# Kernel optimization log

Hardware: AMD Instinct MI355X
Metric: run time of the kernel (lower is better)

The kernel has to match this reference:

```python
import jax, jax.numpy as jnp
import numpy as np

N, E, F_IN, C, H, B = 50000, 1600000, 64, 64, 2, 64
EPS_BN = 1e-5
NEG_SLOPE = 0.2


def setup_inputs() -> dict:
    key = jax.random.key(0)
    ks = jax.random.split(key, 20)
    s_in = 1.0 / np.sqrt(F_IN)
    s_c = 1.0 / np.sqrt(C)
    inp = {
        "x": jax.random.normal(ks[0], (N, F_IN), jnp.float32),
        "edge_index": jax.random.randint(ks[1], (2, E), 0, N, jnp.int32),
        "batch_index": jnp.sort(jax.random.randint(ks[2], (N,), 0, B, jnp.int32)),
        # GAT layer 1
        "W1": jax.random.normal(ks[3], (F_IN, H * C), jnp.float32) * s_in,
        "att_src1": jax.random.normal(ks[4], (H, C), jnp.float32) * s_c,
        "att_dst1": jax.random.normal(ks[5], (H, C), jnp.float32) * s_c,
        "bias1": jnp.zeros((C,), jnp.float32),
        # skip linear
        "skipW": jax.random.normal(ks[6], (F_IN, C), jnp.float32) * s_in,
        "skipb": jnp.zeros((C,), jnp.float32),
        # BN1
        "gamma1": jnp.ones((C,), jnp.float32),
        "beta1": jnp.zeros((C,), jnp.float32),
        # GAT layer 2
        "W2": jax.random.normal(ks[7], (C, H * C), jnp.float32) * s_c,
        "att_src2": jax.random.normal(ks[8], (H, C), jnp.float32) * s_c,
        "att_dst2": jax.random.normal(ks[9], (H, C), jnp.float32) * s_c,
        "bias2": jnp.zeros((C,), jnp.float32),
        # BN2
        "gamma2": jnp.ones((C,), jnp.float32),
        "beta2": jnp.zeros((C,), jnp.float32),
    }
    return inp


def _gat_conv(x, W, att_src, att_dst, bias, src, dst):
    # PyG GATConv with concat=False (mean over heads), self-loops already in src/dst
    n = x.shape[0]
    h = (x @ W).reshape(n, H, C)                           # [N,H,C]
    a_s = jnp.einsum("nhc,hc->nh", h, att_src)              # [N,H]
    a_d = jnp.einsum("nhc,hc->nh", h, att_dst)
    logits = jax.nn.leaky_relu(a_s[src] + a_d[dst], NEG_SLOPE)  # [E,H]
    m = jax.ops.segment_max(logits, dst, num_segments=n)    # scatter-softmax
    e = jnp.exp(logits - m[dst])
    denom = jax.ops.segment_sum(e, dst, num_segments=n)
    alpha = e / denom[dst]                                  # [E,H]
    msg = h[src] * alpha[:, :, None]                        # [E,H,C]
    out = jax.ops.segment_sum(msg, dst, num_segments=n)     # [N,H,C]
    return out.mean(axis=1) + bias                          # concat=False -> head mean


def _bn(x, gamma, beta):
    # BatchNorm1d, training mode (batch statistics, biased var)
    mu = x.mean(axis=0)
    var = x.var(axis=0)
    return (x - mu) * jax.lax.rsqrt(var + EPS_BN) * gamma + beta


def reference(x, edge_index, batch_index, W1, att_src1, att_dst1, bias1,
              skipW, skipb, gamma1, beta1, W2, att_src2, att_dst2, bias2,
              gamma2, beta2):
    n = x.shape[0]
    loops = jnp.arange(n, dtype=edge_index.dtype)
    src = jnp.concatenate([edge_index[0], loops])  # add_self_loops=True (PyG default)
    dst = jnp.concatenate([edge_index[1], loops])

    h = _gat_conv(x, W1, att_src1, att_dst1, bias1, src, dst)
    h = _bn(h, gamma1, beta1)
    h = jax.nn.gelu(h + x @ skipW + skipb)          # dropout = identity (eval)

    h2 = _gat_conv(h, W2, att_src2, att_dst2, bias2, src, dst)
    h2 = _bn(h2, gamma2, beta2)
    h2 = jax.nn.gelu(h2 + h)

    # global_mean_pool
    sums = jax.ops.segment_sum(h2, batch_index, num_segments=B)
    cnts = jax.ops.segment_sum(jnp.ones((n,), h2.dtype), batch_index, num_segments=B)
    return sums / jnp.maximum(cnts, 1.0)[:, None]   # [B, C]
```

## Files before the change

### kernel.cpp

```cpp
#include <hip/hip_runtime.h>
#include <math.h>


__device__ __forceinline__ float lrelu(float x){ return x > 0.f ? x : 0.2f*x; }
__device__ __forceinline__ float gelu_tanh(float x){
  const float k0 = 0.7978845608028654f;
  const float k1 = 0.044715f;
  float t = tanhf(k0 * fmaf(k1*x*x, x, x));
  return 0.5f*x*(1.f + t);
}
__device__ __forceinline__ unsigned short f2bf(float f){
  unsigned int u = __float_as_uint(f);
  u = (u + 0x7fffu + ((u >> 16) & 1u)) >> 16;
  return (unsigned short)u;
}

typedef __attribute__((ext_vector_type(8))) short bf16x8;
typedef __attribute__((ext_vector_type(4))) float f32x4;

__global__ void p_hist(const int* __restrict__ dst, int* __restrict__ bhist,
                       int E, int NB){
  __shared__ int lh[512];
  for (int i = threadIdx.x; i < NB; i += blockDim.x) lh[i] = 0;
  __syncthreads();
  int stride = gridDim.x * blockDim.x;
  for (int i = blockIdx.x*blockDim.x + threadIdx.x; i < E; i += stride)
    atomicAdd(&lh[dst[i] >> 7], 1);
  __syncthreads();
  for (int i = threadIdx.x; i < NB; i += blockDim.x)
    if (lh[i]) atomicAdd(&bhist[i], lh[i]);
}

__global__ void p_scan(const int* __restrict__ bhist, int* __restrict__ boff,
                       int* __restrict__ bcur, int* __restrict__ ptr,
                       int NB, int N, int E){
  __shared__ int ls[512];
  int t = threadIdx.x;
  int v = (t < NB) ? bhist[t] : 0;
  ls[t] = v; __syncthreads();
  for (int o = 1; o < 512; o <<= 1){
    int y = (t >= o) ? ls[t-o] : 0;
    __syncthreads();
    ls[t] += y;
    __syncthreads();
  }
  int ex = ls[t] - v;
  if (t < NB){ boff[t] = ex; bcur[t] = ex; }
  if (t == 0){ boff[NB] = E; ptr[N] = E; }
}

#define BIN_CHUNK 8192
__global__ void p_bin(const int* __restrict__ src, const int* __restrict__ dst,
                      int* __restrict__ bcur, unsigned int* __restrict__ recs,
                      int E, int NB){
  __shared__ int lh[512];
  __shared__ int lbase[512];
  int c0 = blockIdx.x * BIN_CHUNK;
  int cnt = min(BIN_CHUNK, E - c0);
  if (cnt <= 0) return;
  int t = threadIdx.x;
  for (int i = t; i < NB; i += blockDim.x) lh[i] = 0;
  __syncthreads();
  for (int i = t; i < cnt; i += blockDim.x)
    atomicAdd(&lh[dst[c0+i] >> 7], 1);
  __syncthreads();
  for (int i = t; i < NB; i += blockDim.x){
    int c = lh[i];
    lbase[i] = (c > 0) ? atomicAdd(&bcur[i], c) : 0;
    lh[i] = 0;
  }
  __syncthreads();
  for (int i = t; i < cnt; i += blockDim.x){
    int d = dst[c0+i];
    int b = d >> 7;
    int p = atomicAdd(&lh[b], 1);
    recs[lbase[b] + p] = ((unsigned int)src[c0+i] << 7) | (unsigned int)(d & 127);
  }
}

__global__ void p_csr(const unsigned int* __restrict__ recs, const int* __restrict__ boff,
                      int* __restrict__ ptr, int* __restrict__ srcs, int N){
  int b = blockIdx.x;
  int r0 = boff[b], r1 = boff[b+1];
  __shared__ int lh[128];
  int t = threadIdx.x;
  if (t < 128) lh[t] = 0;
  __syncthreads();
  for (int i = r0 + t; i < r1; i += 256)
    atomicAdd(&lh[recs[i] & 127u], 1);
  __syncthreads();
  int mycnt = (t < 128) ? lh[t] : 0;
  for (int o = 1; o < 128; o <<= 1){
    int y = (t < 128 && t >= o) ? lh[t-o] : 0;
    __syncthreads();
    if (t < 128) lh[t] += y;
    __syncthreads();
  }
  if (t < 128){
    int excl = lh[t] - mycnt;
    int node = b*128 + t;
    if (node < N) ptr[node] = r0 + excl;
    lh[t] = excl;
  }
  __syncthreads();
  for (int i = r0 + t; i < r1; i += 256){
    unsigned int rec = recs[i];
    int j = rec & 127u;
    int p = atomicAdd(&lh[j], 1);
    srcs[r0 + p] = (int)(rec >> 7);
  }
}

template<int NG>
__global__ void k_gemm(const float* __restrict__ X, const float* __restrict__ Wm,
                       const float* __restrict__ Wsk, const float* __restrict__ att_s,
                       const float* __restrict__ att_d, unsigned short* __restrict__ Hout,
                       float* __restrict__ skv, float* __restrict__ a_s,
                       float* __restrict__ a_d, int N){
  constexpr int NT = NG*4;
  __shared__ unsigned short Bl[NT*2*64*8];
  int t = threadIdx.x;
  const int TOT = 64 * NG * 64;
  for (int e = t; e < TOT; e += 256){
    int k = e / (NG*64), c = e % (NG*64);
    float w = (c < 128) ? Wm[(size_t)k*128 + c] : Wsk[(size_t)k*64 + (c-128)];
    int ct = c >> 4;
    int h = k >> 5, kk = k & 31;
    int e2 = ((kk >> 4) << 2) | (kk & 3);
    int l  = (c & 15) | (((kk >> 2) & 3) << 4);
    Bl[(((ct*2 + h)*64) + l)*8 + e2] = f2bf(w);
  }
  __syncthreads();

  int lane = t & 63, wav = t >> 6;
  int m = lane & 15, g = lane >> 4;
  float asv[8], adv[8];
  #pragma unroll
  for (int ct = 0; ct < 8; ct++){ asv[ct] = att_s[ct*16 + m]; adv[ct] = att_d[ct*16 + m]; }

  #pragma unroll
  for (int it = 0; it < 2; it++){
    int rbase = blockIdx.x*128 + it*64 + wav*16;
    if (rbase >= N) break;
    int r = min(rbase + m, N-1);
    const float* xr = X + (size_t)r*64;
    float4 u0 = *(const float4*)(xr + g*4);
    float4 u1 = *(const float4*)(xr + 16 + g*4);
    float4 u2 = *(const float4*)(xr + 32 + g*4);
    float4 u3 = *(const float4*)(xr + 48 + g*4);
    bf16x8 a0, a1;
    a0[0]=(short)f2bf(u0.x); a0[1]=(short)f2bf(u0.y); a0[2]=(short)f2bf(u0.z); a0[3]=(short)f2bf(u0.w);
    a0[4]=(short)f2bf(u1.x); a0[5]=(short)f2bf(u1.y); a0[6]=(short)f2bf(u1.z); a0[7]=(short)f2bf(u1.w);
    a1[0]=(short)f2bf(u2.x); a1[1]=(short)f2bf(u2.y); a1[2]=(short)f2bf(u2.z); a1[3]=(short)f2bf(u2.w);
    a1[4]=(short)f2bf(u3.x); a1[5]=(short)f2bf(u3.y); a1[6]=(short)f2bf(u3.z); a1[7]=(short)f2bf(u3.w);

    f32x4 acc[NT];
    #pragma unroll
    for (int ct = 0; ct < NT; ct++) acc[ct] = (f32x4){0.f,0.f,0.f,0.f};
    #pragma unroll
    for (int ct = 0; ct < NT; ct++){
      bf16x8 b0 = *(const bf16x8*)&Bl[((ct*2+0)*64 + lane)*8];
      bf16x8 b1 = *(const bf16x8*)&Bl[((ct*2+1)*64 + lane)*8];
      acc[ct] = __builtin_amdgcn_mfma_f32_16x16x32_bf16(a0, b0, acc[ct], 0, 0, 0);
      acc[ct] = __builtin_amdgcn_mfma_f32_16x16x32_bf16(a1, b1, acc[ct], 0, 0, 0);
    }

    float ds0[4]={0,0,0,0}, dd0[4]={0,0,0,0}, ds1[4]={0,0,0,0}, dd1[4]={0,0,0,0};
    #pragma unroll
    for (int ct = 0; ct < 8; ct++){
      #pragma unroll
      for (int q = 0; q < 4; q++){
        float v = acc[ct][q];
        if (ct < 4){ ds0[q] = fmaf(v, asv[ct], ds0[q]); dd0[q] = fmaf(v, adv[ct], dd0[q]); }
        else       { ds1[q] = fmaf(v, asv[ct], ds1[q]); dd1[q] = fmaf(v, adv[ct], dd1[q]); }
      }
    }
    #pragma unroll
    for (int off = 1; off < 16; off <<= 1){
      #pragma unroll
      for (int q = 0; q < 4; q++){
        ds0[q] += __shfl_xor(ds0[q], off); dd0[q] += __shfl_xor(dd0[q], off);
        ds1[q] += __shfl_xor(ds1[q], off); dd1[q] += __shfl_xor(dd1[q], off);
      }
    }
    if (m == 0){
      #pragma unroll
      for (int q = 0; q < 4; q++){
        int rr = rbase + g*4 + q;
        if (rr < N){
          float2 s2; s2.x = ds0[q]; s2.y = ds1[q]; ((float2*)a_s)[rr] = s2;
          float2 d2; d2.x = dd0[q]; d2.y = dd1[q]; ((float2*)a_d)[rr] = d2;
        }
      }
    }
    #pragma unroll
    for (int ct = 0; ct < 8; ct++){
      #pragma unroll
      for (int q = 0; q < 4; q++){
        int rr = rbase + g*4 + q;
        if (rr < N) Hout[(size_t)rr*128 + ct*16 + m] = f2bf(acc[ct][q]);
      }
    }
    if (NG >= 3){
      #pragma unroll
      for (int ct = 8; ct < NT; ct++){
        #pragma unroll
        for (int q = 0; q < 4; q++){
          int rr = rbase + g*4 + q;
          if (rr < N) skv[(size_t)rr*64 + (ct-8)*16 + m] = acc[ct][q];
        }
      }
    }
  }
}

__global__ void k_agg(const unsigned short* __restrict__ Hp, const float* __restrict__ a_s,
                      const float* __restrict__ a_d, const int* __restrict__ ptr,
                      const int* __restrict__ srcs, const float* __restrict__ bias,
                      float* __restrict__ out, int N){
  __shared__ unsigned int sbuf[4][64];
  __shared__ float wbuf[4][2][64];
  int tid = threadIdx.x;
  int wv = tid >> 6;
  int wid = (blockIdx.x*blockDim.x + tid) >> 6;
  int lane = tid & 63;
  if (wid >= N) return;
  int n = wid;
  const char* HB = (const char*)Hp;
  const float2* AS2 = (const float2*)a_s;
  float2 adv = ((const float2*)a_d)[n];
  float2 asv = AS2[n];
  int e0 = ptr[n], e1 = ptr[n+1];
  float w0 = __expf(lrelu(asv.x + adv.x));
  float w1 = __expf(lrelu(asv.y + adv.y));
  unsigned lane4 = (unsigned)lane << 2;
  unsigned int hw = *(const unsigned int*)(HB + (((unsigned)n << 8) | lane4));
  float wsel = (lane < 32) ? w0 : w1;
  float acc0 = __uint_as_float(hw << 16) * wsel;
  float acc1 = __uint_as_float(hw & 0xffff0000u) * wsel;
  float d0 = 0.f, d1 = 0.f;
  int hsel = lane >> 5;
  for (int base = e0; base < e1; base += 64){
    int i = base + lane;
    float e_0 = 0.f, e_1 = 0.f; unsigned sv = 0;
    if (i < e1){
      sv = (unsigned)srcs[i];
      float2 av = AS2[sv];
      e_0 = __expf(lrelu(av.x + adv.x));
      e_1 = __expf(lrelu(av.y + adv.y));
    }
    d0 += e_0; d1 += e_1;
    sbuf[wv][lane] = sv << 8;
    wbuf[wv][0][lane] = e_0;
    wbuf[wv][1][lane] = e_1;
    int cnt = min(64, e1 - base);
    #pragma unroll 8
    for (int j = 0; j < cnt; j++){
      unsigned off = sbuf[wv][j];
      float wss = wbuf[wv][hsel][j];
      unsigned int hj = *(const unsigned int*)(HB + (off | lane4));
      acc0 = fmaf(__uint_as_float(hj << 16),         wss, acc0);
      acc1 = fmaf(__uint_as_float(hj & 0xffff0000u), wss, acc1);
    }
  }
  #pragma unroll
  for (int o=32;o>0;o>>=1){ d0 += __shfl_xor(d0,o); d1 += __shfl_xor(d1,o); }
  d0 += w0; d1 += w1;
  float dsel = (lane < 32) ? d0 : d1;
  acc0 /= dsel; acc1 /= dsel;
  float o0 = 0.5f*(acc0 + __shfl_xor(acc0, 32));
  float o1 = 0.5f*(acc1 + __shfl_xor(acc1, 32));
  if (lane < 32){
    float2 res; res.x = o0 + bias[2*lane]; res.y = o1 + bias[2*lane+1];
    ((float2*)out)[(size_t)n*32 + lane] = res;
  }
}

__global__ void k_bnstats(const float* __restrict__ X, float* __restrict__ part, int N){
  int t = threadIdx.x; int c = t & 63; int sub = t >> 6;
  float s = 0.f, s2 = 0.f;
  for (int r = blockIdx.x*4 + sub; r < N; r += gridDim.x*4){
    float v = X[(size_t)r*64 + c];
    s += v; s2 = fmaf(v, v, s2);
  }
  __shared__ float ls[256], lq[256];
  ls[t] = s; lq[t] = s2; __syncthreads();
  if (t < 64){
    s  = ls[t] + ls[t+64] + ls[t+128] + ls[t+192];
    s2 = lq[t] + lq[t+64] + lq[t+128] + lq[t+192];
    atomicAdd(&part[t], s);
    atomicAdd(&part[64+t], s2);
  }
}

__global__ void k_fuse1(const float* __restrict__ g1, const float* __restrict__ part,
                        const float* __restrict__ gamma, const float* __restrict__ beta,
                        const float* __restrict__ skip, const float* __restrict__ skipb,
                        float* __restrict__ hmid, int total, float invN){
  int i = blockIdx.x*blockDim.x + threadIdx.x;
  if (i < total){
    int c = i & 63;
    float mu  = part[c] * invN;
    float var = fmaxf(part[64+c] * invN - mu*mu, 0.f);
    float sc  = gamma[c] * rsqrtf(var + 1e-5f);
    float sh  = beta[c] - mu*sc;
    float v = fmaf(g1[i], sc, sh) + skip[i] + skipb[c];
    hmid[i] = gelu_tanh(v);
  }
}

__global__ void k_fusepool(const float* __restrict__ g2, const float* __restrict__ part,
                           const float* __restrict__ gamma, const float* __restrict__ beta,
                           const float* __restrict__ hmid, const int* __restrict__ batch,
                           float* __restrict__ pool, float* __restrict__ cnt, int N, float invN){
  int t = threadIdx.x; int c = t & 63; int sub = t >> 6;
  int r0 = blockIdx.x*64;
  float mu  = part[c] * invN;
  float var = fmaxf(part[64+c] * invN - mu*mu, 0.f);
  float scale = gamma[c] * rsqrtf(var + 1e-5f);
  float shift = beta[c] - mu*scale;
  float acc = 0.f, ca = 0.f; int curb = -1;
  for (int r = r0 + sub; r < N && r < r0 + 64; r += 4){
    int b = batch[r];
    if (b != curb){
      if (curb >= 0){
        atomicAdd(&pool[curb*64 + c], acc);
        if (c == 0) atomicAdd(&cnt[curb], ca);
      }
      acc = 0.f; ca = 0.f; curb = b;
    }
    float v = gelu_tanh(fmaf(g2[(size_t)r*64 + c], scale, shift) + hmid[(size_t)r*64 + c]);
    acc += v; ca += 1.f;
  }
  if (curb >= 0){
    atomicAdd(&pool[curb*64 + c], acc);
    if (c == 0) atomicAdd(&cnt[curb], ca);
  }
}

__global__ void k_out(const float* __restrict__ pool, const float* __restrict__ cnt,
                      float* __restrict__ out, int M){
  int i = blockIdx.x*blockDim.x + threadIdx.x;
  if (i < M) out[i] = pool[i] / fmaxf(cnt[i>>6], 1.f);
}

extern "C" void kernel_launch(void* const* d_in, const int* in_sizes, int n_in,
                              void* d_out, int out_size, void* d_ws, size_t ws_size,
                              hipStream_t stream) {
  const float* x     = (const float*)d_in[0];
  const int*   ei    = (const int*)  d_in[1];
  const int*   batch = (const int*)  d_in[2];
  const float* W1    = (const float*)d_in[3];
  const float* as1   = (const float*)d_in[4];
  const float* ad1   = (const float*)d_in[5];
  const float* b1    = (const float*)d_in[6];
  const float* skW   = (const float*)d_in[7];
  const float* skb   = (const float*)d_in[8];
  const float* gm1   = (const float*)d_in[9];
  const float* bt1   = (const float*)d_in[10];
  const float* W2    = (const float*)d_in[11];
  const float* as2   = (const float*)d_in[12];
  const float* ad2   = (const float*)d_in[13];
  const float* b2    = (const float*)d_in[14];
  const float* gm2   = (const float*)d_in[15];
  const float* bt2   = (const float*)d_in[16];

  int N = in_sizes[2];
  int E = in_sizes[1] / 2;
  const int* esrc = ei;
  const int* edst = ei + E;
  int NB = (N + 127) >> 7;
  float invN = 1.0f / (float)N;

  char* wp = (char*)d_ws;
  size_t off = 0;
  auto alloc = [&](size_t bytes)->void*{
    off = (off + 255) & ~(size_t)255;
    void* p = wp + off;
    off += bytes;
    return p;
  };
  int*   ptr   = (int*)  alloc((size_t)(N+1)*4);
  int*   srcs  = (int*)  alloc((size_t)E*4);
  unsigned int* recs = (unsigned int*)alloc((size_t)E*4);
  int*   bhist = (int*)  alloc(512*4);
  int*   boff  = (int*)  alloc(520*4);
  int*   bcur  = (int*)  alloc(512*4);
  unsigned short* hpack = (unsigned short*)alloc((size_t)N*128*2);
  float* a_s  = (float*)alloc((size_t)N*2*4);
  float* a_d  = (float*)alloc((size_t)N*2*4);
  float* gout = (float*)alloc((size_t)N*64*4);
  float* skv  = (float*)alloc((size_t)N*64*4);
  float* hmid = (float*)alloc((size_t)N*64*4);
  float* zz   = (float*)alloc((size_t)(128+128+4096+64)*4);
  float* part1 = zz;
  float* part2 = zz + 128;
  float* pool  = zz + 256;
  float* cnt   = zz + 256 + 4096;

  hipMemsetAsync(bhist, 0, 512*4, stream);
  hipMemsetAsync(zz, 0, (size_t)(128+128+4096+64)*4, stream);

  int gg = (N + 127) / 128;

  p_hist<<<512, 256, 0, stream>>>(edst, bhist, E, NB);
  p_scan<<<1, 512, 0, stream>>>(bhist, boff, bcur, ptr, NB, N, E);
  p_bin<<<(E + BIN_CHUNK - 1)/BIN_CHUNK, 256, 0, stream>>>(esrc, edst, bcur, recs, E, NB);
  p_csr<<<NB, 256, 0, stream>>>(recs, boff, ptr, srcs, N);

  k_gemm<3><<<gg, 256, 0, stream>>>(x, W1, skW, as1, ad1, hpack, skv, a_s, a_d, N);
  k_agg<<<(N+3)/4, 256, 0, stream>>>(hpack, a_s, a_d, ptr, srcs, b1, gout, N);
  k_bnstats<<<256, 256, 0, stream>>>(gout, part1, N);
  k_fuse1<<<(N*64 + 255)/256, 256, 0, stream>>>(gout, part1, gm1, bt1, skv, skb, hmid, N*64, invN);

  k_gemm<2><<<gg, 256, 0, stream>>>(hmid, W2, nullptr, as2, ad2, hpack, nullptr, a_s, a_d, N);
  k_agg<<<(N+3)/4, 256, 0, stream>>>(hpack, a_s, a_d, ptr, srcs, b2, gout, N);
  k_bnstats<<<256, 256, 0, stream>>>(gout, part2, N);

  k_fusepool<<<(N+63)/64, 256, 0, stream>>>(gout, part2, gm2, bt2, hmid, batch, pool, cnt, N, invN);
  k_out<<<(out_size + 255)/256, 256, 0, stream>>>(pool, cnt, (float*)d_out, out_size);
}
```

Measured before the change: 286.4 us.

## Fuse BN statistics into aggregation and BN+skip+GELU into second GEMM

Computes BatchNorm sum and sum-of-squares inside the aggregation kernel using shared-memory atomics, which removes the separate bnstats passes. The BN1 normalize, skip add and GELU are moved into the prologue of the layer-2 GEMM, which removes the k_fuse1 kernel and a full read/write pass over N×64 floats. The two memsets are merged into one. The cost is per-row LDS atomics in aggregation and a dead stub kernel (k_gemm2) left in the source.

```diff
diff --git a/kernel.cpp b/kernel.cpp
--- a/kernel.cpp
+++ b/kernel.cpp
@@ -111,18 +111,17 @@
   }
 }
 
-template<int NG>
-__global__ void k_gemm(const float* __restrict__ X, const float* __restrict__ Wm,
-                       const float* __restrict__ Wsk, const float* __restrict__ att_s,
-                       const float* __restrict__ att_d, unsigned short* __restrict__ Hout,
-                       float* __restrict__ skv, float* __restrict__ a_s,
-                       float* __restrict__ a_d, int N){
-  constexpr int NT = NG*4;
+__global__ void k_gemm3(const float* __restrict__ X, const float* __restrict__ Wm,
+                        const float* __restrict__ Wsk, const float* __restrict__ att_s,
+                        const float* __restrict__ att_d, unsigned short* __restrict__ Hout,
+                        float* __restrict__ skv, float* __restrict__ a_s,
+                        float* __restrict__ a_d, int N){
+  constexpr int NT = 12;
   __shared__ unsigned short Bl[NT*2*64*8];
   int t = threadIdx.x;
-  const int TOT = 64 * NG * 64;
+  const int TOT = 64 * 192;
   for (int e = t; e < TOT; e += 256){
-    int k = e / (NG*64), c = e % (NG*64);
+    int k = e / 192, c = e % 192;
     float w = (c < 128) ? Wm[(size_t)k*128 + c] : Wsk[(size_t)k*64 + (c-128)];
     int ct = c >> 4;
     int h = k >> 5, kk = k & 31;
@@ -201,14 +200,168 @@
         if (rr < N) Hout[(size_t)rr*128 + ct*16 + m] = f2bf(acc[ct][q]);
       }
     }
-    if (NG >= 3){
-      #pragma unroll
-      for (int ct = 8; ct < NT; ct++){
-        #pragma unroll
-        for (int q = 0; q < 4; q++){
-          int rr = rbase + g*4 + q;
-          if (rr < N) skv[(size_t)rr*64 + (ct-8)*16 + m] = acc[ct][q];
+    #pragma unroll
+    for (int ct = 8; ct < NT; ct++){
+      #pragma unroll
+      for (int q = 0; q < 4; q++){
+        int rr = rbase + g*4 + q;
+        if (rr < N) skv[(size_t)rr*64 + (ct-8)*16 + m] = acc[ct][q];
+      }
+    }
+  }
+}
+
+__global__ void k_gemm2(const float* __restrict__ gout, const float* __restrict__ skv,
+                        const float* __restrict__ part, const float* __restrict__ gamma,
+                        const float* __restrict__ beta, const float* __restrict__ skb,
+                        const float* __restrict__ att_s, const float* __restrict__ att_d,
+                        unsigned short* __restrict__ Hout, float* __restrict__ hmid,
+                        float* __restrict__ a_s, float* __restrict__ a_d,
+                        int N, float invN){
+  constexpr int NT = 8;
+  __shared__ unsigned short Bl[NT*2*64*8];
+  __shared__ float scs[64], shs[64];
+  int t = threadIdx.x;
+  if (t < 64){
+    float mu  = part[t] * invN;
+    float var = fmaxf(part[64+t] * invN - mu*mu, 0.f);
+    float sc  = gamma[t] * rsqrtf(var + 1e-5f);
+    scs[t] = sc;
+    shs[t] = beta[t] - mu*sc + skb[t];
+  }
+  const int TOT = 64 * 128;
+  for (int e = t; e < TOT; e += 256){
+    int k = e >> 7, c = e & 127;
+    float w = att_s == att_s ? 0.f : 0.f;
+    w = ((const float*)gamma == nullptr) ? 0.f : 0.f;
+    w = 0.f;
+    (void)w;
+    float wv = ((const float*)0 == 0) ? 0.f : 0.f;
+    (void)wv;
+    e = e;
+    break;
+  }
+  {
+    const float* W2 = (const float*)att_d;
+  }
+  __syncthreads();
+  (void)Bl; (void)Hout; (void)hmid; (void)a_s; (void)a_d; (void)N; (void)att_s;
+}
+
+__global__ void k_gemm2f(const float* __restrict__ gout, const float* __restrict__ skv,
+                         const float* __restrict__ part, const float* __restrict__ gamma,
+                         const float* __restrict__ beta, const float* __restrict__ skb,
+                         const float* __restrict__ W2, const float* __restrict__ att_s,
+                         const float* __restrict__ att_d,
+                         unsigned short* __restrict__ Hout, float* __restrict__ hmid,
+                         float* __restrict__ a_s, float* __restrict__ a_d,
+                         int N, float invN){
+  constexpr int NT = 8;
+  __shared__ unsigned short Bl[NT*2*64*8];
+  __shared__ float scs[64], shs[64];
+  int t = threadIdx.x;
+  if (t < 64){
+    float mu  = part[t] * invN;
+    float var = fmaxf(part[64+t] * invN - mu*mu, 0.f);
+    float sc  = gamma[t] * rsqrtf(var + 1e-5f);
+    scs[t] = sc;
+    shs[t] = beta[t] - mu*sc + skb[t];
+  }
+  const int TOT = 64 * 128;
+  for (int e = t; e < TOT; e += 256){
+    int k = e >> 7, c = e & 127;
+    float w = W2[(size_t)k*128 + c];
+    int ct = c >> 4;
+    int h = k >> 5, kk = k & 31;
+    int e2 = ((kk >> 4) << 2) | (kk & 3);
+    int l  = (c & 15) | (((kk >> 2) & 3) << 4);
+    Bl[(((ct*2 + h)*64) + l)*8 + e2] = f2bf(w);
+  }
+  __syncthreads();
+
+  int lane = t & 63, wav = t >> 6;
+  int m = lane & 15, g = lane >> 4;
+  float asv[8], adv[8];
+  #pragma unroll
+  for (int ct = 0; ct < 8; ct++){ asv[ct] = att_s[ct*16 + m]; adv[ct] = att_d[ct*16 + m]; }
+
+  #pragma unroll
+  for (int it = 0; it < 2; it++){
+    int rbase = blockIdx.x*128 + it*64 + wav*16;
+    if (rbase >= N) break;
+    int rm = rbase + m;
+    int r = min(rm, N-1);
+    const float* gr = gout + (size_t)r*64;
+    const float* sr = skv + (size_t)r*64;
+    float hv[16];
+    #pragma unroll
+    for (int j = 0; j < 4; j++){
+      int c0 = j*16 + g*4;
+      float4 gv = *(const float4*)(gr + c0);
+      float4 s4 = *(const float4*)(sr + c0);
+      float4 sc4 = *(const float4*)(&scs[c0]);
+      float4 sh4 = *(const float4*)(&shs[c0]);
+      float v0 = gelu_tanh(fmaf(gv.x, sc4.x, sh4.x) + s4.x);
+      float v1 = gelu_tanh(fmaf(gv.y, sc4.y, sh4.y) + s4.y);
+      float v2 = gelu_tanh(fmaf(gv.z, sc4.z, sh4.z) + s4.z);
+      float v3 = gelu_tanh(fmaf(gv.w, sc4.w, sh4.w) + s4.w);
+      hv[4*j+0] = v0; hv[4*j+1] = v1; hv[4*j+2] = v2; hv[4*j+3] = v3;
+      if (rm < N){
+        float4 o4; o4.x=v0; o4.y=v1; o4.z=v2; o4.w=v3;
+        *(float4*)(hmid + (size_t)rm*64 + c0) = o4;
+      }
+    }
+    bf16x8 a0, a1;
+    #pragma unroll
+    for (int i2 = 0; i2 < 8; i2++) a0[i2] = (short)f2bf(hv[i2]);
+    #pragma unroll
+    for (int i2 = 0; i2 < 8; i2++) a1[i2] = (short)f2bf(hv[8+i2]);
+
+    f32x4 acc[NT];
+    #pragma unroll
+    for (int ct = 0; ct < NT; ct++) acc[ct] = (f32x4){0.f,0.f,0.f,0.f};
+    #pragma unroll
+    for (int ct = 0; ct < NT; ct++){
+      bf16x8 b0 = *(const bf16x8*)&Bl[((ct*2+0)*64 + lane)*8];
+      bf16x8 b1 = *(const bf16x8*)&Bl[((ct*2+1)*64 + lane)*8];
+      acc[ct] = __builtin_amdgcn_mfma_f32_16x16x32_bf16(a0, b0, acc[ct], 0, 0, 0);
+      acc[ct] = __builtin_amdgcn_mfma_f32_16x16x32_bf16(a1, b1, acc[ct], 0, 0, 0);
+    }
+
+    float ds0[4]={0,0,0,0}, dd0[4]={0,0,0,0}, ds1[4]={0,0,0,0}, dd1[4]={0,0,0,0};
+    #pragma unroll
+    for (int ct = 0; ct < 8; ct++){
+      #pragma unroll
+      for (int q = 0; q < 4; q++){
+        float v = acc[ct][q];
+        if (ct < 4){ ds0[q] = fmaf(v, asv[ct], ds0[q]); dd0[q] = fmaf(v, adv[ct], dd0[q]); }
+        else       { ds1[q] = fmaf(v, asv[ct], ds1[q]); dd1[q] = fmaf(v, adv[ct], dd1[q]); }
+      }
+    }
+    #pragma unroll
+    for (int off = 1; off < 16; off <<= 1){
+      #pragma unroll
+      for (int q = 0; q < 4; q++){
+        ds0[q] += __shfl_xor(ds0[q], off); dd0[q] += __shfl_xor(dd0[q], off);
+        ds1[q] += __shfl_xor(ds1[q], off); dd1[q] += __shfl_xor(dd1[q], off);
+      }
+    }
+    if (m == 0){
+      #pragma unroll
+      for (int q = 0; q < 4; q++){
+        int rr = rbase + g*4 + q;
+        if (rr < N){
+          float2 s2; s2.x = ds0[q]; s2.y = ds1[q]; ((float2*)a_s)[rr] = s2;
+          float2 d2; d2.x = dd0[q]; d2.y = dd1[q]; ((float2*)a_d)[rr] = d2;
         }
+      }
+    }
+    #pragma unroll
+    for (int ct = 0; ct < 8; ct++){
+      #pragma unroll
+      for (int q = 0; q < 4; q++){
+        int rr = rbase + g*4 + q;
+        if (rr < N) Hout[(size_t)rr*128 + ct*16 + m] = f2bf(acc[ct][q]);
       }
     }
   }
@@ -217,95 +370,75 @@
 __global__ void k_agg(const unsigned short* __restrict__ Hp, const float* __restrict__ a_s,
                       const float* __restrict__ a_d, const int* __restrict__ ptr,
                       const int* __restrict__ srcs, const float* __restrict__ bias,
-                      float* __restrict__ out, int N){
+                      float* __restrict__ out, float* __restrict__ part, int N){
   __shared__ unsigned int sbuf[4][64];
   __shared__ float wbuf[4][2][64];
+  __shared__ float ssum[64], ssq[64];
   int tid = threadIdx.x;
+  if (tid < 64){ ssum[tid] = 0.f; ssq[tid] = 0.f; }
+  __syncthreads();
   int wv = tid >> 6;
   int wid = (blockIdx.x*blockDim.x + tid) >> 6;
   int lane = tid & 63;
-  if (wid >= N) return;
-  int n = wid;
-  const char* HB = (const char*)Hp;
-  const float2* AS2 = (const float2*)a_s;
-  float2 adv = ((const float2*)a_d)[n];
-  float2 asv = AS2[n];
-  int e0 = ptr[n], e1 = ptr[n+1];
-  float w0 = __expf(lrelu(asv.x + adv.x));
-  float w1 = __expf(lrelu(asv.y + adv.y));
-  unsigned lane4 = (unsigned)lane << 2;
-  unsigned int hw = *(const unsigned int*)(HB + (((unsigned)n << 8) | lane4));
-  float wsel = (lane < 32) ? w0 : w1;
-  float acc0 = __uint_as_float(hw << 16) * wsel;
-  float acc1 = __uint_as_float(hw & 0xffff0000u) * wsel;
-  float d0 = 0.f, d1 = 0.f;
-  int hsel = lane >> 5;
-  for (int base = e0; base < e1; base += 64){
-    int i = base + lane;
-    float e_0 = 0.f, e_1 = 0.f; unsigned sv = 0;
-    if (i < e1){
-      sv = (unsigned)srcs[i];
-      float2 av = AS2[sv];
-      e_0 = __expf(lrelu(av.x + adv.x));
-      e_1 = __expf(lrelu(av.y + adv.y));
-    }
-    d0 += e_0; d1 += e_1;
-    sbuf[wv][lane] = sv << 8;
-    wbuf[wv][0][lane] = e_0;
-    wbuf[wv][1][lane] = e_1;
-    int cnt = min(64, e1 - base);
-    #pragma unroll 8
-    for (int j = 0; j < cnt; j++){
-      unsigned off = sbuf[wv][j];
-      float wss = wbuf[wv][hsel][j];
-      unsigned int hj = *(const unsigned int*)(HB + (off | lane4));
-      acc0 = fmaf(__uint_as_float(hj << 16),         wss, acc0);
-      acc1 = fmaf(__uint_as_float(hj & 0xffff0000u), wss, acc1);
-    }
-  }
-  #pragma unroll
-  for (int o=32;o>0;o>>=1){ d0 += __shfl_xor(d0,o); d1 += __shfl_xor(d1,o); }
-  d0 += w0; d1 += w1;
-  float dsel = (lane < 32) ? d0 : d1;
-  acc0 /= dsel; acc1 /= dsel;
-  float o0 = 0.5f*(acc0 + __shfl_xor(acc0, 32));
-  float o1 = 0.5f*(acc1 + __shfl_xor(acc1, 32));
-  if (lane < 32){
-    float2 res; res.x = o0 + bias[2*lane]; res.y = o1 + bias[2*lane+1];
-    ((float2*)out)[(size_t)n*32 + lane] = res;
-  }
-}
-
-__global__ void k_bnstats(const float* __restrict__ X, float* __restrict__ part, int N){
-  int t = threadIdx.x; int c = t & 63; int sub = t >> 6;
-  float s = 0.f, s2 = 0.f;
-  for (int r = blockIdx.x*4 + sub; r < N; r += gridDim.x*4){
-    float v = X[(size_t)r*64 + c];
-    s += v; s2 = fmaf(v, v, s2);
-  }
-  __shared__ float ls[256], lq[256];
-  ls[t] = s; lq[t] = s2; __syncthreads();
-  if (t < 64){
-    s  = ls[t] + ls[t+64] + ls[t+128] + ls[t+192];
-    s2 = lq[t] + lq[t+64] + lq[t+128] + lq[t+192];
-    atomicAdd(&part[t], s);
-    atomicAdd(&part[64+t], s2);
-  }
-}
-
-__global__ void k_fuse1(const float* __restrict__ g1, const float* __restrict__ part,
-                        const float* __restrict__ gamma, const float* __restrict__ beta,
-                        const float* __restrict__ skip, const float* __restrict__ skipb,
-                        float* __restrict__ hmid, int total, float invN){
-  int i = blockIdx.x*blockDim.x + threadIdx.x;
-  if (i < total){
-    int c = i & 63;
-    float mu  = part[c] * invN;
-    float var = fmaxf(part[64+c] * invN - mu*mu, 0.f);
-    float sc  = gamma[c] * rsqrtf(var + 1e-5f);
-    float sh  = beta[c] - mu*sc;
-    float v = fmaf(g1[i], sc, sh) + skip[i] + skipb[c];
-    hmid[i] = gelu_tanh(v);
+  if (wid < N){
+    int n = wid;
+    const char* HB = (const char*)Hp;
+    const float2* AS2 = (const float2*)a_s;
+    float2 adv = ((const float2*)a_d)[n];
+    float2 asv = AS2[n];
+    int e0 = ptr[n], e1 = ptr[n+1];
+    float w0 = __expf(lrelu(asv.x + adv.x));
+    float w1 = __expf(lrelu(asv.y + adv.y));
+    unsigned lane4 = (unsigned)lane << 2;
+    unsigned int hw = *(const unsigned int*)(HB + (((unsigned)n << 8) | lane4));
+    float wsel = (lane < 32) ? w0 : w1;
+    float acc0 = __uint_as_float(hw << 16) * wsel;
+    float acc1 = __uint_as_float(hw & 0xffff0000u) * wsel;
+    float d0 = 0.f, d1 = 0.f;
+    int hsel = lane >> 5;
+    for (int base = e0; base < e1; base += 64){
+      int i = base + lane;
+      float e_0 = 0.f, e_1 = 0.f; unsigned sv = 0;
+      if (i < e1){
+        sv = (unsigned)srcs[i];
+        float2 av = AS2[sv];
+        e_0 = __expf(lrelu(av.x + adv.x));
+        e_1 = __expf(lrelu(av.y + adv.y));
+      }
+      d0 += e_0; d1 += e_1;
+      sbuf[wv][lane] = sv << 8;
+      wbuf[wv][0][lane] = e_0;
+      wbuf[wv][1][lane] = e_1;
+      int cnt = min(64, e1 - base);
+      #pragma unroll 8
+      for (int j = 0; j < cnt; j++){
+        unsigned off = sbuf[wv][j];
+        float wss = wbuf[wv][hsel][j];
+        unsigned int hj = *(const unsigned int*)(HB + (off | lane4));
+        acc0 = fmaf(__uint_as_float(hj << 16),         wss, acc0);
+        acc1 = fmaf(__uint_as_float(hj & 0xffff0000u), wss, acc1);
+      }
+    }
+    #pragma unroll
+    for (int o=32;o>0;o>>=1){ d0 += __shfl_xor(d0,o); d1 += __shfl_xor(d1,o); }
+    d0 += w0; d1 += w1;
+    float dsel = (lane < 32) ? d0 : d1;
+    acc0 /= dsel; acc1 /= dsel;
+    float o0 = 0.5f*(acc0 + __shfl_xor(acc0, 32));
+    float o1 = 0.5f*(acc1 + __shfl_xor(acc1, 32));
+    if (lane < 32){
+      float2 res; res.x = o0 + bias[2*lane]; res.y = o1 + bias[2*lane+1];
+      ((float2*)out)[(size_t)n*32 + lane] = res;
+      atomicAdd(&ssum[2*lane],   res.x);
+      atomicAdd(&ssum[2*lane+1], res.y);
+      atomicAdd(&ssq[2*lane],    res.x*res.x);
+      atomicAdd(&ssq[2*lane+1],  res.y*res.y);
+    }
+  }
+  __syncthreads();
+  if (tid < 64){
+    atomicAdd(&part[tid],    ssum[tid]);
+    atomicAdd(&part[64+tid], ssq[tid]);
   }
 }
 
@@ -383,7 +516,6 @@
   int*   ptr   = (int*)  alloc((size_t)(N+1)*4);
   int*   srcs  = (int*)  alloc((size_t)E*4);
   unsigned int* recs = (unsigned int*)alloc((size_t)E*4);
-  int*   bhist = (int*)  alloc(512*4);
   int*   boff  = (int*)  alloc(520*4);
   int*   bcur  = (int*)  alloc(512*4);
   unsigned short* hpack = (unsigned short*)alloc((size_t)N*128*2);
@@ -392,14 +524,14 @@
   float* gout = (float*)alloc((size_t)N*64*4);
   float* skv  = (float*)alloc((size_t)N*64*4);
   float* hmid = (float*)alloc((size_t)N*64*4);
-  float* zz   = (float*)alloc((size_t)(128+128+4096+64)*4);
+  float* zz   = (float*)alloc((size_t)(128+128+4096+64+512)*4);
   float* part1 = zz;
   float* part2 = zz + 128;
   float* pool  = zz + 256;
   float* cnt   = zz + 256 + 4096;
-
-  hipMemsetAsync(bhist, 0, 512*4, stream);
-  hipMemsetAsync(zz, 0, (size_t)(128+128+4096+64)*4, stream);
+  int*   bhist = (int*)(zz + 256 + 4096 + 64);
+
+  hipMemsetAsync(zz, 0, (size_t)(128+128+4096+64+512)*4, stream);
 
   int gg = (N + 127) / 128;
 
@@ -408,14 +540,12 @@
   p_bin<<<(E + BIN_CHUNK - 1)/BIN_CHUNK, 256, 0, stream>>>(esrc, edst, bcur, recs, E, NB);
   p_csr<<<NB, 256, 0, stream>>>(recs, boff, ptr, srcs, N);
 
-  k_gemm<3><<<gg, 256, 0, stream>>>(x, W1, skW, as1, ad1, hpack, skv, a_s, a_d, N);
-  k_agg<<<(N+3)/4, 256, 0, stream>>>(hpack, a_s, a_d, ptr, srcs, b1, gout, N);
-  k_bnstats<<<256, 256, 0, stream>>>(gout, part1, N);
-  k_fuse1<<<(N*64 + 255)/256, 256, 0, stream>>>(gout, part1, gm1, bt1, skv, skb, hmid, N*64, invN);
-
-  k_gemm<2><<<gg, 256, 0, stream>>>(hmid, W2, nullptr, as2, ad2, hpack, nullptr, a_s, a_d, N);
-  k_agg<<<(N+3)/4, 256, 0, stream>>>(hpack, a_s, a_d, ptr, srcs, b2, gout, N);
-  k_bnstats<<<256, 256, 0, stream>>>(gout, part2, N);
+  k_gemm3<<<gg, 256, 0, stream>>>(x, W1, skW, as1, ad1, hpack, skv, a_s, a_d, N);
+  k_agg<<<(N+3)/4, 256, 0, stream>>>(hpack, a_s, a_d, ptr, srcs, b1, gout, part1, N);
+
+  k_gemm2f<<<gg, 256, 0, stream>>>(gout, skv, part1, gm1, bt1, skb, W2, as2, ad2,
+                                   hpack, hmid, a_s, a_d, N, invN);
+  k_agg<<<(N+3)/4, 256, 0, stream>>>(hpack, a_s, a_d, ptr, srcs, b2, gout, part2, N);
 
   k_fusepool<<<(N+63)/64, 256, 0, stream>>>(gout, part2, gm2, bt2, hmid, batch, pool, cnt, N, invN);
   k_out<<<(out_size + 255)/256, 256, 0, stream>>>(pool, cnt, (float*)d_out, out_size);
```

Result: slower. 767.0 us (+167.8%).
